# Kernel tuning notes

Hardware: AMD Instinct MI355X
Metric: run time of the kernel (lower is better)

Reference implementation:

```python
import jax, jax.numpy as jnp
import numpy as np

N_NODES = 50000
N_EDGES = 1_600_000
D_IN = 128
D_OUT = 128


def setup_inputs() -> dict:
    key = jax.random.key(0)
    k1, k2, k3, k4 = jax.random.split(key, 4)
    x = jax.random.normal(k1, (N_NODES, D_IN), dtype=jnp.float32)
    weight = jax.random.normal(k2, (D_IN, D_OUT), dtype=jnp.float32)
    bias = jnp.zeros((D_OUT,), dtype=jnp.float32)
    edge_row = jax.random.randint(k3, (N_EDGES,), 0, N_NODES, dtype=jnp.int64 if jax.config.jax_enable_x64 else jnp.int32)
    edge_col = jax.random.randint(k4, (N_EDGES,), 0, N_NODES, dtype=jnp.int64 if jax.config.jax_enable_x64 else jnp.int32)
    return {"x": x, "weight": weight, "bias": bias, "edge_row": edge_row, "edge_col": edge_col}


def reference(x, weight, bias, edge_row, edge_col):
    # edges_sparse is a binary [N, N] COO adjacency; edge (row=i, col=j) has value 1.
    n = x.shape[0]
    ones = jnp.ones(edge_row.shape[0], dtype=x.dtype)
    # out_degree = A.sum(dim=1): row sums of the adjacency
    out_degree = jax.ops.segment_sum(ones, edge_row, num_segments=n)
    deg_inv_sqrt = out_degree ** -0.5  # D = diag(deg^-0.5)
    # (D A D) x  ==  scatter_i sum_j deg_i^-0.5 * deg_j^-0.5 * x_j over edges (i, j)
    w = deg_inv_sqrt[edge_row] * deg_inv_sqrt[edge_col]  # [E]
    msg = w[:, None] * x[edge_col]                        # [E, D_IN]
    agg = jax.ops.segment_sum(msg, edge_row, num_segments=n)  # [N, D_IN]
    # dense projection + bias
    return agg @ weight + bias
```

## Files before the change

kernel.cpp:

```cpp
#include <hip/hip_runtime.h>
#include <hip/hip_bf16.h>

#define NODES   50000
#define EDGES   1600000
#define DIM     128
#define NB      391
#define BSTRIDE 4608
#define TILE    8192
#define EPT     32
#define NTILES  196
#define ZROW    50000

typedef unsigned int   u32;
typedef unsigned short u16;
typedef __attribute__((ext_vector_type(4))) float f32x4;
typedef __attribute__((ext_vector_type(8))) short s16x8;

__device__ inline u16 f2bf(float f) {
  __hip_bfloat16 h = __float2bfloat16(f);
  return *reinterpret_cast<u16*>(&h);
}

__global__ __launch_bounds__(256) void k_prep(const float* __restrict__ W,
                                              u16* __restrict__ wts,
                                              int* __restrict__ gcursor) {
  __shared__ float T[32 * 132];
  int t = threadIdx.x;
  int gi = blockIdx.x * 256 + t;
  if (gi < NB) gcursor[gi] = gi * BSTRIDE;
  int c0 = blockIdx.x * 32;
#pragma unroll
  for (int i = 0; i < 16; ++i) {
    int idx = i * 256 + t;
    int k = idx >> 5;
    int cc = idx & 31;
    T[cc * 132 + k] = W[k * 128 + c0 + cc];
  }
  __syncthreads();
#pragma unroll
  for (int i = 0; i < 2; ++i) {
    int idx = i * 256 + t;
    int cc = idx >> 4;
    int kc = idx & 15;
    int c = c0 + cc;
    int kbase = kc * 8;
    u32 p[4];
#pragma unroll
    for (int u = 0; u < 4; ++u) {
      float a = T[cc * 132 + kbase + 2 * u];
      float b = T[cc * 132 + kbase + 2 * u + 1];
      p[u] = (u32)f2bf(a) | ((u32)f2bf(b) << 16);
    }
    int off = c * 256 + ((kbase * 2) ^ ((c & 15) << 4));
    *(uint4*)((char*)wts + off) = make_uint4(p[0], p[1], p[2], p[3]);
  }
}

__global__ __launch_bounds__(256) void k_binA(const int* __restrict__ erow,
                                              const int* __restrict__ ecol,
                                              int* __restrict__ gcursor,
                                              u32* __restrict__ binned) {
  __shared__ int hist[NB];
  __shared__ int lcur[NB];
  int t = threadIdx.x;
  for (int b = t; b < NB; b += 256) hist[b] = 0;
  __syncthreads();
  int base = blockIdx.x * TILE;
  u32 v[EPT];
#pragma unroll
  for (int k = 0; k < 8; ++k) {
    int e4 = base + k * 1024 + t * 4;
    if (e4 < EDGES) {
      int4 rr = *(const int4*)&erow[e4];
      int4 cc = *(const int4*)&ecol[e4];
      v[k * 4 + 0] = ((u32)rr.x << 16) | (u32)cc.x;
      v[k * 4 + 1] = ((u32)rr.y << 16) | (u32)cc.y;
      v[k * 4 + 2] = ((u32)rr.z << 16) | (u32)cc.z;
      v[k * 4 + 3] = ((u32)rr.w << 16) | (u32)cc.w;
      atomicAdd(&hist[(u32)rr.x >> 7], 1);
      atomicAdd(&hist[(u32)rr.y >> 7], 1);
      atomicAdd(&hist[(u32)rr.z >> 7], 1);
      atomicAdd(&hist[(u32)rr.w >> 7], 1);
    } else {
      v[k * 4 + 0] = 0xffffffffu;
      v[k * 4 + 1] = 0xffffffffu;
      v[k * 4 + 2] = 0xffffffffu;
      v[k * 4 + 3] = 0xffffffffu;
    }
  }
  __syncthreads();
  for (int b = t; b < NB; b += 256) {
    int h = hist[b];
    lcur[b] = h ? atomicAdd(&gcursor[b], h) : 0;
  }
  __syncthreads();
#pragma unroll
  for (int k = 0; k < EPT; ++k) {
    if (v[k] != 0xffffffffu) {
      int b = (int)(v[k] >> 23);
      int pos = atomicAdd(&lcur[b], 1);
      if (pos < (b + 1) * BSTRIDE) binned[pos] = v[k];
    }
  }
}

__global__ __launch_bounds__(256) void k_binB(const u32* __restrict__ binned,
                                              const int* __restrict__ gcur,
                                              int2* __restrict__ rp2,
                                              float* __restrict__ dis,
                                              u16* __restrict__ cols) {
  __shared__ int cnt[128];
  __shared__ int sc[128];
  __shared__ int lcur[128];
  __shared__ u16 stage[BSTRIDE];
  int b = blockIdx.x;
  int t = threadIdx.x;
  int n0 = b << 7;
  int s = b * BSTRIDE;
  int e = gcur[b];
  if (e > s + BSTRIDE) e = s + BSTRIDE;
  int cntE = e - s;
  if (t < 128) cnt[t] = 0;
  __syncthreads();
  u32 held[18];
#pragma unroll
  for (int k = 0; k < 18; ++k) {
    int j = s + t + k * 256;
    u32 v = (j < e) ? binned[j] : 0xffffffffu;
    held[k] = v;
    if (v != 0xffffffffu) atomicAdd(&cnt[(int)(v >> 16) - n0], 1);
  }
  __syncthreads();
  if (t < 128) sc[t] = cnt[t];
  __syncthreads();
  for (int off = 1; off < 128; off <<= 1) {
    int tmp = (t >= off && t < 128) ? sc[t - off] : 0;
    __syncthreads();
    if (t < 128) sc[t] += tmp;
    __syncthreads();
  }
  if (t < 128) {
    int n = n0 + t;
    if (n < NODES) {
      int lexcl = sc[t] - cnt[t];
      rp2[n] = make_int2(s + lexcl, s + lexcl + cnt[t]);
      lcur[t] = lexcl;
      dis[n] = rsqrtf((float)cnt[t]);
    }
  }
  __syncthreads();
#pragma unroll
  for (int k = 0; k < 18; ++k) {
    u32 v = held[k];
    if (v != 0xffffffffu) {
      int pos = atomicAdd(&lcur[(int)(v >> 16) - n0], 1);
      stage[pos] = (u16)(v & 0xffffu);
    }
  }
  __syncthreads();
  {
    u32* dst = (u32*)(cols + s);
    const u32* src = (const u32*)stage;
    int nw = (cntE + 1) >> 1;
    for (int i = t; i < nw; i += 256) dst[i] = src[i];
  }
}

__global__ __launch_bounds__(256) void k_gemm(const float* __restrict__ x,
                                              const u16* __restrict__ wts,
                                              const float* __restrict__ dis,
                                              u16* __restrict__ y2) {
  __shared__ u16 xs[64 * 128];
  __shared__ u16 ws[128 * 128];
  const int t = threadIdx.x;
  const int bb = blockIdx.x * 64;

  {
    const uint4* src = (const uint4*)wts;
    uint4* dst = (uint4*)ws;
#pragma unroll
    for (int i = 0; i < 8; ++i) dst[i * 256 + t] = src[i * 256 + t];
  }
  {
#pragma unroll
    for (int i = 0; i < 8; ++i) {
      int goff = i * 4096 + t * 16;
      int row = goff >> 9;
      int gr = bb + row;
      float4 v = make_float4(0.f, 0.f, 0.f, 0.f);
      if (gr < NODES) v = *(const float4*)((const char*)x + (size_t)gr * 512 + (goff & 511));
      u32 lo = (u32)f2bf(v.x) | ((u32)f2bf(v.y) << 16);
      u32 hi = (u32)f2bf(v.z) | ((u32)f2bf(v.w) << 16);
      int colb = (goff & 511) >> 1;
      int off = row * 256 + (colb ^ ((row & 15) << 4));
      *(uint2*)((char*)xs + off) = make_uint2(lo, hi);
    }
  }
  __syncthreads();

  const int w = t >> 6, l = t & 63, m = l & 15, g = l >> 4;
  f32x4 acc[8];
#pragma unroll
  for (int j = 0; j < 8; ++j) acc[j] = (f32x4)0.0f;

  const char* xb = (const char*)xs;
  const char* wb = (const char*)ws;
  const int arow = w * 16 + m;
#pragma unroll
  for (int s = 0; s < 4; ++s) {
    int kx = (g * 16 + s * 64) ^ (m << 4);
    s16x8 a = *(const s16x8*)(xb + arow * 256 + kx);
#pragma unroll
    for (int j = 0; j < 8; ++j) {
      s16x8 b = *(const s16x8*)(wb + (j * 16 + m) * 256 + kx);
      acc[j] = __builtin_amdgcn_mfma_f32_16x16x32_bf16(a, b, acc[j], 0, 0, 0);
    }
  }

  int rbase = bb + w * 16 + g * 4;
  float4 d4 = *(const float4*)&dis[rbase];
#pragma unroll
  for (int j = 0; j < 8; ++j) {
#pragma unroll
    for (int r = 0; r < 4; ++r) {
      int gr = rbase + r;
      float dv = (r == 0) ? d4.x : (r == 1) ? d4.y : (r == 2) ? d4.z : d4.w;
      float val = (gr < NODES) ? acc[j][r] * dv : 0.0f;
      y2[(size_t)gr * 128 + j * 16 + m] = f2bf(val);
    }
  }
}

__global__ __launch_bounds__(256) void k_agg(const u16* __restrict__ y2,
                                             const int2* __restrict__ rp2,
                                             const u16* __restrict__ cols,
                                             const float* __restrict__ dis,
                                             const float* __restrict__ bias,
                                             float* __restrict__ out) {
  int node = (blockIdx.x * 256 + threadIdx.x) >> 6;
  int l = threadIdx.x & 63;
  if (node >= NODES) return;
  int q = l >> 4;
  int m = l & 15;
  int2 rr = rp2[node];
  int s = rr.x;
  int e = rr.y;

  float a0 = 0.f, a1 = 0.f, a2 = 0.f, a3 = 0.f;
  float a4 = 0.f, a5 = 0.f, a6 = 0.f, a7 = 0.f;
  const uint4* yb = (const uint4*)y2;

  int c0 = (s + q      < e) ? (int)cols[s + q]      : ZROW;
  int c1 = (s + 4 + q  < e) ? (int)cols[s + 4 + q]  : ZROW;
  int c2 = (s + 8 + q  < e) ? (int)cols[s + 8 + q]  : ZROW;
  int c3 = (s + 12 + q < e) ? (int)cols[s + 12 + q] : ZROW;

  for (int jb = s; jb < e; jb += 16) {
    int nb = jb + 16;
    int d0 = (nb + q      < e) ? (int)cols[nb + q]      : ZROW;
    int d1 = (nb + 4 + q  < e) ? (int)cols[nb + 4 + q]  : ZROW;
    int d2 = (nb + 8 + q  < e) ? (int)cols[nb + 8 + q]  : ZROW;
    int d3 = (nb + 12 + q < e) ? (int)cols[nb + 12 + q] : ZROW;
    uint4 v0 = yb[c0 * 16 + m];
    uint4 v1 = yb[c1 * 16 + m];
    uint4 v2 = yb[c2 * 16 + m];
    uint4 v3 = yb[c3 * 16 + m];
#define ACC(v)                                   \
    a0 += __uint_as_float((v).x << 16);          \
    a1 += __uint_as_float((v).x & 0xffff0000u);  \
    a2 += __uint_as_float((v).y << 16);          \
    a3 += __uint_as_float((v).y & 0xffff0000u);  \
    a4 += __uint_as_float((v).z << 16);          \
    a5 += __uint_as_float((v).z & 0xffff0000u);  \
    a6 += __uint_as_float((v).w << 16);          \
    a7 += __uint_as_float((v).w & 0xffff0000u);
    ACC(v0) ACC(v1) ACC(v2) ACC(v3)
#undef ACC
    c0 = d0; c1 = d1; c2 = d2; c3 = d3;
  }

  a0 += __shfl_xor(a0, 16); a0 += __shfl_xor(a0, 32);
  a1 += __shfl_xor(a1, 16); a1 += __shfl_xor(a1, 32);
  a2 += __shfl_xor(a2, 16); a2 += __shfl_xor(a2, 32);
  a3 += __shfl_xor(a3, 16); a3 += __shfl_xor(a3, 32);
  a4 += __shfl_xor(a4, 16); a4 += __shfl_xor(a4, 32);
  a5 += __shfl_xor(a5, 16); a5 += __shfl_xor(a5, 32);
  a6 += __shfl_xor(a6, 16); a6 += __shfl_xor(a6, 32);
  a7 += __shfl_xor(a7, 16); a7 += __shfl_xor(a7, 32);

  float di = (e > s) ? dis[node] : 0.0f;
  if (q < 2) {
    float r0 = q ? a4 : a0;
    float r1 = q ? a5 : a1;
    float r2 = q ? a6 : a2;
    float r3 = q ? a7 : a3;
    float4 bb = *(const float4*)&bias[m * 8 + q * 4];
    f32x4 o;
    o[0] = bb.x + di * r0;
    o[1] = bb.y + di * r1;
    o[2] = bb.z + di * r2;
    o[3] = bb.w + di * r3;
    __builtin_nontemporal_store(o, (f32x4*)&out[(size_t)node * 128 + m * 8 + q * 4]);
  }
}

extern "C" void kernel_launch(void* const* d_in, const int* in_sizes, int n_in,
                              void* d_out, int out_size, void* d_ws, size_t ws_size,
                              hipStream_t stream) {
  const float* x    = (const float*)d_in[0];
  const float* W    = (const float*)d_in[1];
  const float* bias = (const float*)d_in[2];
  const int*   erow = (const int*)d_in[3];
  const int*   ecol = (const int*)d_in[4];
  float* out = (float*)d_out;

  char* ws = (char*)d_ws;
  int*   gcursor = (int*)(ws + 0);
  int2*  rp2     = (int2*)(ws + 4096);
  float* dis     = (float*)(ws + 409600);
  u16*   wts     = (u16*)(ws + 614400);
  u32*   binned  = (u32*)(ws + 655360);
  u16*   cols    = (u16*)(ws + 7864320);
  u16*   y2      = (u16*)(ws + 11468800);

  k_prep<<<4, 256, 0, stream>>>(W, wts, gcursor);
  k_binA<<<NTILES, 256, 0, stream>>>(erow, ecol, gcursor, binned);
  k_binB<<<NB, 256, 0, stream>>>(binned, gcursor, rp2, dis, cols);
  k_gemm<<<(NODES + 63) / 64, 256, 0, stream>>>(x, wts, dis, y2);
  k_agg<<<(NODES * 64 + 255) / 256, 256, 0, stream>>>(y2, rp2, cols, dis, bias, out);
}
```

Baseline: 93.85 us.

## Fuse weight prep into binning and GEMM into bin-finalize kernel

```diff
diff --git a/kernel.cpp b/kernel.cpp
--- a/kernel.cpp
+++ b/kernel.cpp
@@ -21,48 +21,47 @@
   return *reinterpret_cast<u16*>(&h);
 }
 
-__global__ __launch_bounds__(256) void k_prep(const float* __restrict__ W,
-                                              u16* __restrict__ wts,
-                                              int* __restrict__ gcursor) {
-  __shared__ float T[32 * 132];
-  int t = threadIdx.x;
-  int gi = blockIdx.x * 256 + t;
-  if (gi < NB) gcursor[gi] = gi * BSTRIDE;
-  int c0 = blockIdx.x * 32;
-#pragma unroll
-  for (int i = 0; i < 16; ++i) {
-    int idx = i * 256 + t;
-    int k = idx >> 5;
-    int cc = idx & 31;
-    T[cc * 132 + k] = W[k * 128 + c0 + cc];
-  }
-  __syncthreads();
-#pragma unroll
-  for (int i = 0; i < 2; ++i) {
-    int idx = i * 256 + t;
-    int cc = idx >> 4;
-    int kc = idx & 15;
-    int c = c0 + cc;
-    int kbase = kc * 8;
-    u32 p[4];
-#pragma unroll
-    for (int u = 0; u < 4; ++u) {
-      float a = T[cc * 132 + kbase + 2 * u];
-      float b = T[cc * 132 + kbase + 2 * u + 1];
-      p[u] = (u32)f2bf(a) | ((u32)f2bf(b) << 16);
-    }
-    int off = c * 256 + ((kbase * 2) ^ ((c & 15) << 4));
-    *(uint4*)((char*)wts + off) = make_uint4(p[0], p[1], p[2], p[3]);
-  }
-}
-
 __global__ __launch_bounds__(256) void k_binA(const int* __restrict__ erow,
                                               const int* __restrict__ ecol,
+                                              const float* __restrict__ W,
+                                              u16* __restrict__ wts,
                                               int* __restrict__ gcursor,
                                               u32* __restrict__ binned) {
   __shared__ int hist[NB];
   __shared__ int lcur[NB];
+  __shared__ float T[32 * 132];
   int t = threadIdx.x;
+
+  if (blockIdx.x < 4) {
+    int c0 = blockIdx.x * 32;
+#pragma unroll
+    for (int i = 0; i < 16; ++i) {
+      int idx = i * 256 + t;
+      int k = idx >> 5;
+      int cc = idx & 31;
+      T[cc * 132 + k] = W[k * 128 + c0 + cc];
+    }
+    __syncthreads();
+#pragma unroll
+    for (int i = 0; i < 2; ++i) {
+      int idx = i * 256 + t;
+      int cc = idx >> 4;
+      int kc = idx & 15;
+      int c = c0 + cc;
+      int kbase = kc * 8;
+      u32 p[4];
+#pragma unroll
+      for (int u = 0; u < 4; ++u) {
+        float a = T[cc * 132 + kbase + 2 * u];
+        float b = T[cc * 132 + kbase + 2 * u + 1];
+        p[u] = (u32)f2bf(a) | ((u32)f2bf(b) << 16);
+      }
+      int off = c * 256 + ((kbase * 2) ^ ((c & 15) << 4));
+      *(uint4*)((char*)wts + off) = make_uint4(p[0], p[1], p[2], p[3]);
+    }
+    __syncthreads();
+  }
+
   for (int b = t; b < NB; b += 256) hist[b] = 0;
   __syncthreads();
   int base = blockIdx.x * TILE;
@@ -91,7 +90,7 @@
   __syncthreads();
   for (int b = t; b < NB; b += 256) {
     int h = hist[b];
-    lcur[b] = h ? atomicAdd(&gcursor[b], h) : 0;
+    lcur[b] = h ? (b * BSTRIDE + atomicAdd(&gcursor[b], h)) : 0;
   }
   __syncthreads();
 #pragma unroll
@@ -104,22 +103,29 @@
   }
 }
 
-__global__ __launch_bounds__(256) void k_binB(const u32* __restrict__ binned,
-                                              const int* __restrict__ gcur,
-                                              int2* __restrict__ rp2,
-                                              float* __restrict__ dis,
-                                              u16* __restrict__ cols) {
+__global__ __launch_bounds__(256) void k_bg(const u32* __restrict__ binned,
+                                            const int* __restrict__ gcur,
+                                            const float* __restrict__ x,
+                                            const u16* __restrict__ wts,
+                                            int2* __restrict__ rp2,
+                                            float* __restrict__ dis,
+                                            u16* __restrict__ cols,
+                                            u16* __restrict__ y2) {
   __shared__ int cnt[128];
   __shared__ int sc[128];
   __shared__ int lcur[128];
-  __shared__ u16 stage[BSTRIDE];
-  int b = blockIdx.x;
-  int t = threadIdx.x;
-  int n0 = b << 7;
-  int s = b * BSTRIDE;
-  int e = gcur[b];
-  if (e > s + BSTRIDE) e = s + BSTRIDE;
-  int cntE = e - s;
+  __shared__ float disl[128];
+  __shared__ u16 ws_[128 * 128];
+  __shared__ u16 xs_[64 * 128];
+  u16* stage = ws_;
+
+  const int b = blockIdx.x, t = threadIdx.x;
+  const int n0 = b << 7;
+  const int s = b * BSTRIDE;
+  int cntE = gcur[b];
+  if (cntE > BSTRIDE) cntE = BSTRIDE;
+  const int e = s + cntE;
+
   if (t < 128) cnt[t] = 0;
   __syncthreads();
   u32 held[18];
@@ -140,12 +146,13 @@
     __syncthreads();
   }
   if (t < 128) {
+    disl[t] = rsqrtf((float)cnt[t]);
     int n = n0 + t;
     if (n < NODES) {
       int lexcl = sc[t] - cnt[t];
       rp2[n] = make_int2(s + lexcl, s + lexcl + cnt[t]);
       lcur[t] = lexcl;
-      dis[n] = rsqrtf((float)cnt[t]);
+      dis[n] = disl[t];
     }
   }
   __syncthreads();
@@ -164,24 +171,21 @@
     int nw = (cntE + 1) >> 1;
     for (int i = t; i < nw; i += 256) dst[i] = src[i];
   }
-}
-
-__global__ __launch_bounds__(256) void k_gemm(const float* __restrict__ x,
-                                              const u16* __restrict__ wts,
-                                              const float* __restrict__ dis,
-                                              u16* __restrict__ y2) {
-  __shared__ u16 xs[64 * 128];
-  __shared__ u16 ws[128 * 128];
-  const int t = threadIdx.x;
-  const int bb = blockIdx.x * 64;
+  __syncthreads();
 
   {
     const uint4* src = (const uint4*)wts;
-    uint4* dst = (uint4*)ws;
+    uint4* dst = (uint4*)ws_;
 #pragma unroll
     for (int i = 0; i < 8; ++i) dst[i * 256 + t] = src[i * 256 + t];
   }
-  {
+  const int w = t >> 6, l = t & 63, m = l & 15, g = l >> 4;
+  const char* xb = (const char*)xs_;
+  const char* wb = (const char*)ws_;
+
+#pragma unroll
+  for (int tile = 0; tile < 2; ++tile) {
+    const int bb = n0 + tile * 64;
 #pragma unroll
     for (int i = 0; i < 8; ++i) {
       int goff = i * 4096 + t * 16;
@@ -193,41 +197,37 @@
       u32 hi = (u32)f2bf(v.z) | ((u32)f2bf(v.w) << 16);
       int colb = (goff & 511) >> 1;
       int off = row * 256 + (colb ^ ((row & 15) << 4));
-      *(uint2*)((char*)xs + off) = make_uint2(lo, hi);
-    }
-  }
-  __syncthreads();
-
-  const int w = t >> 6, l = t & 63, m = l & 15, g = l >> 4;
-  f32x4 acc[8];
-#pragma unroll
-  for (int j = 0; j < 8; ++j) acc[j] = (f32x4)0.0f;
-
-  const char* xb = (const char*)xs;
-  const char* wb = (const char*)ws;
-  const int arow = w * 16 + m;
-#pragma unroll
-  for (int s = 0; s < 4; ++s) {
-    int kx = (g * 16 + s * 64) ^ (m << 4);
-    s16x8 a = *(const s16x8*)(xb + arow * 256 + kx);
+      *(uint2*)((char*)xs_ + off) = make_uint2(lo, hi);
+    }
+    __syncthreads();
+
+    f32x4 acc[8];
+#pragma unroll
+    for (int j = 0; j < 8; ++j) acc[j] = (f32x4)0.0f;
+    const int arow = w * 16 + m;
+#pragma unroll
+    for (int ss = 0; ss < 4; ++ss) {
+      int kx = (g * 16 + ss * 64) ^ (m << 4);
+      s16x8 a = *(const s16x8*)(xb + arow * 256 + kx);
+#pragma unroll
+      for (int j = 0; j < 8; ++j) {
+        s16x8 bv = *(const s16x8*)(wb + (j * 16 + m) * 256 + kx);
+        acc[j] = __builtin_amdgcn_mfma_f32_16x16x32_bf16(a, bv, acc[j], 0, 0, 0);
+      }
+    }
+
+    int rbase = bb + w * 16 + g * 4;
+    int lbase = rbase - n0;
 #pragma unroll
     for (int j = 0; j < 8; ++j) {
-      s16x8 b = *(const s16x8*)(wb + (j * 16 + m) * 256 + kx);
-      acc[j] = __builtin_amdgcn_mfma_f32_16x16x32_bf16(a, b, acc[j], 0, 0, 0);
-    }
-  }
-
-  int rbase = bb + w * 16 + g * 4;
-  float4 d4 = *(const float4*)&dis[rbase];
-#pragma unroll
-  for (int j = 0; j < 8; ++j) {
-#pragma unroll
-    for (int r = 0; r < 4; ++r) {
-      int gr = rbase + r;
-      float dv = (r == 0) ? d4.x : (r == 1) ? d4.y : (r == 2) ? d4.z : d4.w;
-      float val = (gr < NODES) ? acc[j][r] * dv : 0.0f;
-      y2[(size_t)gr * 128 + j * 16 + m] = f2bf(val);
-    }
+#pragma unroll
+      for (int r = 0; r < 4; ++r) {
+        int gr = rbase + r;
+        float val = (gr < NODES) ? acc[j][r] * disl[lbase + r] : 0.0f;
+        y2[(size_t)gr * 128 + j * 16 + m] = f2bf(val);
+      }
+    }
+    __syncthreads();
   }
 }
 
@@ -323,9 +323,8 @@
   u16*   cols    = (u16*)(ws + 7864320);
   u16*   y2      = (u16*)(ws + 11468800);
 
-  k_prep<<<4, 256, 0, stream>>>(W, wts, gcursor);
-  k_binA<<<NTILES, 256, 0, stream>>>(erow, ecol, gcursor, binned);
-  k_binB<<<NB, 256, 0, stream>>>(binned, gcursor, rp2, dis, cols);
-  k_gemm<<<(NODES + 63) / 64, 256, 0, stream>>>(x, wts, dis, y2);
+  hipMemsetAsync(gcursor, 0, NB * sizeof(int), stream);
+  k_binA<<<NTILES, 256, 0, stream>>>(erow, ecol, W, wts, gcursor, binned);
+  k_bg<<<NB, 256, 0, stream>>>(binned, gcursor, x, wts, rp2, dis, cols, y2);
   k_agg<<<(NODES * 64 + 255) / 256, 256, 0, stream>>>(y2, rp2, cols, dis, bias, out);
 }
```

Result: no change. 94.02 us (+0.2%).
